# Optimization experiments

Measured on AMD Instinct MI355X. Metric: run time of the kernel, lower is better.

The kernel has to match this reference:

```python
import jax, jax.numpy as jnp
import numpy as np

B, T = 32, 128
D_PATCH, D_PLM, H, P = 128, 768, 4, 64
HD = D_PLM // H          # head_dim = 192
N_TOK = 15               # 1+1+4+4+4+1 patch tokens
EPS = 1e-5


def layernorm(x, g, b):
    m = jnp.mean(x, axis=-1, keepdims=True)
    v = jnp.var(x, axis=-1, keepdims=True)
    return (x - m) * jax.lax.rsqrt(v + EPS) * g + b


def setup_inputs() -> dict:
    key = jax.random.key(0)
    ks = jax.random.split(key, 12)
    nrm = lambda k, shp, s: jax.random.normal(k, shp, jnp.float32) * s
    return {
        "state":    jax.random.normal(ks[0], (B, T, 6, 6), jnp.float32),
        # per-feature patch embedders: scalar feats (0,1,5) in_dim=1, windowed feats (2,3,4) in_dim=3
        "w_scalar": nrm(ks[1], (3, 1, D_PATCH), 0.5),
        "b_scalar": jnp.zeros((3, D_PATCH), jnp.float32),
        "w_patch":  nrm(ks[2], (3, 3, D_PATCH), 0.3),
        "b_patch":  jnp.zeros((3, D_PATCH), jnp.float32),
        "feat_emb": nrm(ks[3], (6, D_PATCH), 0.02),
        "pn_g": jnp.ones((D_PATCH,), jnp.float32),
        "pn_b": jnp.zeros((D_PATCH,), jnp.float32),
        "wq": nrm(ks[4], (D_PATCH, D_PLM), 0.05), "bq": jnp.zeros((D_PLM,), jnp.float32),
        "wk": nrm(ks[5], (D_PLM, D_PLM), 0.02),   "bk": jnp.zeros((D_PLM,), jnp.float32),
        "wv": nrm(ks[6], (D_PLM, D_PLM), 0.02),   "bv": jnp.zeros((D_PLM,), jnp.float32),
        "wp": nrm(ks[7], (D_PATCH, D_PLM), 0.05), "bp": jnp.zeros((D_PLM,), jnp.float32),
        "wo": nrm(ks[8], (D_PLM, D_PLM), 0.02),   "bo": jnp.zeros((D_PLM,), jnp.float32),
        "on_g": jnp.ones((D_PLM,), jnp.float32),
        "on_b": jnp.zeros((D_PLM,), jnp.float32),
        # text prototype bank (rows sampled from word embedding table in the original)
        "protos": nrm(ks[9], (P, D_PLM), 1.0),
    }


def reference(state, w_scalar, b_scalar, w_patch, b_patch, feat_emb, pn_g, pn_b,
              wq, bq, wk, bk, wv, bv, wp, bp, wo, bo, on_g, on_b, protos):
    b, t = state.shape[0], state.shape[1]
    s = state.reshape(b * t, 6, 6)                       # (N,6,6)
    N = s.shape[0]

    # scalar features 0,1,5: last timestep, patch_size=1 -> 1 token each
    sc = s[:, jnp.array([0, 1, 5]), -1]                  # (N,3)
    sc_emb = sc[..., None] * w_scalar[:, 0][None] + b_scalar[None]   # (N,3,Dp)
    sc_emb = sc_emb + feat_emb[jnp.array([0, 1, 5])][None]

    # windowed features 2,3,4: length 6, patch_len 3, stride 1 -> 4 tokens each
    pf = s[:, jnp.array([2, 3, 4]), :]                   # (N,3,6)
    win = jnp.stack([pf[..., i:i + 3] for i in range(4)], axis=2)    # (N,3,4,3)
    p_emb = jnp.einsum('nfkp,fpd->nfkd', win, w_patch) + b_patch[None, :, None]
    p_emb = p_emb + feat_emb[jnp.array([2, 3, 4])][None, :, None]

    # concat in feature order 0,1,2,3,4,5 -> (N,15,Dp), then LayerNorm
    pe = jnp.concatenate([sc_emb[:, 0:1], sc_emb[:, 1:2],
                          p_emb[:, 0], p_emb[:, 1], p_emb[:, 2],
                          sc_emb[:, 2:3]], axis=1)
    pe = layernorm(pe, pn_g, pn_b)

    # cross-attention: Q from patches, K/V from 64 text prototypes
    q = (pe @ wq + bq).reshape(N, N_TOK, H, HD)
    k = (protos @ wk + bk).reshape(P, H, HD)
    v = (protos @ wv + bv).reshape(P, H, HD)
    scores = jnp.einsum('nthd,phd->nhtp', q, k) / np.float32(np.sqrt(HD))
    attn = jax.nn.softmax(scores, axis=-1)               # (N,H,T,P)
    rep = jnp.einsum('nhtp,phd->nthd', attn, v).reshape(N, N_TOK, D_PLM)

    out = (rep @ wo + bo) + (pe @ wp + bp)               # dual projection residual
    out = layernorm(out, on_g, on_b)
    return out.reshape(b, t, N_TOK, D_PLM)
```

## Files before the change

kernel.cpp:

```cpp
#include <hip/hip_runtime.h>

#define NTOK 15
#define DP   128
#define DM   768
#define NH   4
#define HD   192
#define NP   64
#define EPSF 1e-5f
#define KW2  384

typedef __attribute__((ext_vector_type(8))) short bf16x8;
typedef __attribute__((ext_vector_type(4))) float f32x4;
typedef __attribute__((ext_vector_type(4))) unsigned short us4;

__device__ __forceinline__ unsigned short f2bf(float x) {
    unsigned u = __float_as_uint(x);
    u = (u + 0x7FFF + ((u >> 16) & 1)) >> 16;
    return (unsigned short)u;
}
__device__ __forceinline__ int swzP(int row, int b) { return row * 256 + (b ^ ((row & 7) << 4)); }
__device__ __forceinline__ int swzB(int row, int b) { return row * 512 + (b ^ ((row & 7) << 4)); }

__global__ __launch_bounds__(192) void kv_kernel(
    const float* __restrict__ protos,
    const float* __restrict__ wk, const float* __restrict__ bk,
    const float* __restrict__ wv, const float* __restrict__ bv,
    float* __restrict__ Kraw, float* __restrict__ Vf)
{
    int r  = blockIdx.x >> 2;
    int jc = blockIdx.x & 3;
    int j  = jc * 192 + threadIdx.x;
    __shared__ float prow[DM];
    for (int i = threadIdx.x; i < DM; i += 192) prow[i] = protos[r * DM + i];
    __syncthreads();
    float aK = bk[j], aV = bv[j];
    for (int d = 0; d < DM; ++d) {
        float p = prow[d];
        aK += p * wk[d * DM + j];
        aV += p * wv[d * DM + j];
    }
    int h = j / HD, jj = j - h * HD;
    Kraw[(h * NP + r) * HD + jj] = aK;
    Vf[r * DM + j] = aV;
}

__global__ __launch_bounds__(256) void fold_kernel(
    const float* __restrict__ Kraw, const float* __restrict__ Vf,
    const float* __restrict__ wq, const float* __restrict__ bq,
    const float* __restrict__ wo, const float* __restrict__ wp,
    unsigned short* __restrict__ KWb, float* __restrict__ kqb,
    unsigned short* __restrict__ Wcat)
{
    int b = blockIdx.x, tid = threadIdx.x;
    if (b >= 256) {
        int idx = (b - 256) * 256 + tid;
        int j = idx >> 7, d = idx & 127;
        Wcat[(size_t)j * KW2 + 256 + d] = f2bf(wp[d * DM + j]);
        return;
    }
    int hp = b, h = hp >> 6, p = hp & 63;
    __shared__ float Kl[HD], Vl[HD];
    if (tid < HD) {
        Kl[tid] = Kraw[hp * HD + tid];
        Vl[tid] = Vf[p * DM + h * HD + tid];
    }
    __syncthreads();
    const float scale = 0.07216878364870323f;
    if (tid < DP) {
        float a = 0.f;
        for (int l = 0; l < HD; ++l) a += wq[tid * DM + h * HD + l] * Kl[l];
        KWb[hp * DP + tid] = f2bf(scale * a);
    } else if (tid == DP) {
        float a = 0.f;
        for (int l = 0; l < HD; ++l) a += bq[h * HD + l] * Kl[l];
        kqb[hp] = scale * a;
    }
    for (int jj = 0; jj < 3; ++jj) {
        int j = jj * 256 + tid;
        float a = 0.f;
        for (int l = 0; l < HD; ++l) a += wo[(h * HD + l) * DM + j] * Vl[l];
        Wcat[(size_t)j * KW2 + hp] = f2bf(a);
    }
}

__global__ __launch_bounds__(256, 4) void phaseA_kernel(
    const float* __restrict__ state,
    const float* __restrict__ w_scalar, const float* __restrict__ b_scalar,
    const float* __restrict__ w_patch,  const float* __restrict__ b_patch,
    const float* __restrict__ feat_emb,
    const float* __restrict__ pn_g, const float* __restrict__ pn_b,
    const unsigned short* __restrict__ KWb, const float* __restrict__ kqb,
    unsigned short* __restrict__ abufG, int Nrows)
{
    int tid = threadIdx.x;
    int w = tid >> 6, lane = tid & 63;
    int kg = lane >> 4, lr = lane & 15;
    int nb = blockIdx.x;
    size_t rowbase = (size_t)nb * 32;

    __shared__ float peF[32 * DP];
    __shared__ __align__(16) char pebf[32 * 256];
    __shared__ float srow[72];

    if (tid < 72) {
        int rr = tid / 36;
        int gr = nb * 2 + rr;
        srow[tid] = (gr < Nrows) ? state[(size_t)gr * 36 + (tid - rr * 36)] : 0.f;
    }
    __syncthreads();

    #pragma unroll
    for (int it = 0; it < 16; ++it) {
        int idx = it * 256 + tid;
        int row = idx >> 7, d = idx & 127;
        int t = row & 15;
        const float* sr = &srow[(row >> 4) * 36];
        float val;
        if (t == 15) {
            val = 0.f;
        } else if (t == 0) {
            val = sr[5]  * w_scalar[0 * DP + d] + b_scalar[0 * DP + d] + feat_emb[0 * DP + d];
        } else if (t == 1) {
            val = sr[11] * w_scalar[1 * DP + d] + b_scalar[1 * DP + d] + feat_emb[1 * DP + d];
        } else if (t == 14) {
            val = sr[35] * w_scalar[2 * DP + d] + b_scalar[2 * DP + d] + feat_emb[5 * DP + d];
        } else {
            int f = (t - 2) / 4;
            int k = (t - 2) % 4;
            const float* pr = &sr[(2 + f) * 6];
            float acc = b_patch[f * DP + d] + feat_emb[(2 + f) * DP + d];
            for (int p = 0; p < 3; ++p) acc += pr[k + p] * w_patch[(f * 3 + p) * DP + d];
            val = acc;
        }
        peF[row * DP + d] = val;
    }
    __syncthreads();

    {
        int g = tid >> 3, ln = tid & 7;
        int t = g & 15;
        int gr = nb * 2 + (g >> 4);
        if (t == 15 || gr >= Nrows) {
            for (int d = ln; d < DP; d += 8)
                *(unsigned short*)(pebf + swzP(g, d * 2)) = 0;
        } else {
            float s = 0.f, s2 = 0.f;
            for (int d = ln; d < DP; d += 8) { float x = peF[g * DP + d]; s += x; s2 += x * x; }
            for (int off = 4; off; off >>= 1) {
                s  += __shfl_xor(s,  off, 64);
                s2 += __shfl_xor(s2, off, 64);
            }
            float m   = s / DP;
            float var = s2 / DP - m * m;
            float rin = 1.0f / sqrtf(var + EPSF);
            for (int d = ln; d < DP; d += 8) {
                float x = (peF[g * DP + d] - m) * rin * pn_g[d] + pn_b[d];
                *(unsigned short*)(pebf + swzP(g, d * 2)) = f2bf(x);
            }
        }
    }
    __syncthreads();

    {
        const int h = w;
        const unsigned short* kwh = KWb + (size_t)h * NP * DP;
        bf16x8 ka[4][4];
        float4 kqv[4];
        #pragma unroll
        for (int Mt = 0; Mt < 4; ++Mt) {
            #pragma unroll
            for (int kk = 0; kk < 4; ++kk)
                ka[Mt][kk] = *(const bf16x8*)(kwh + (Mt * 16 + lr) * DP + kk * 32 + kg * 8);
            kqv[Mt] = *(const float4*)(kqb + h * 64 + Mt * 16 + kg * 4);
        }
        #pragma unroll
        for (int Ntl = 0; Ntl < 2; ++Ntl) {
            bf16x8 qb[4];
            #pragma unroll
            for (int kk = 0; kk < 4; ++kk)
                qb[kk] = *(const bf16x8*)(pebf + swzP(Ntl * 16 + lr, (kk * 32 + kg * 8) * 2));
            f32x4 sacc[4];
            #pragma unroll
            for (int Mt = 0; Mt < 4; ++Mt) sacc[Mt] = (f32x4){0.f, 0.f, 0.f, 0.f};
            #pragma unroll
            for (int kk = 0; kk < 4; ++kk)
                #pragma unroll
                for (int Mt = 0; Mt < 4; ++Mt)
                    sacc[Mt] = __builtin_amdgcn_mfma_f32_16x16x32_bf16(ka[Mt][kk], qb[kk], sacc[Mt], 0, 0, 0);
            #pragma unroll
            for (int Mt = 0; Mt < 4; ++Mt) {
                sacc[Mt][0] += kqv[Mt].x; sacc[Mt][1] += kqv[Mt].y;
                sacc[Mt][2] += kqv[Mt].z; sacc[Mt][3] += kqv[Mt].w;
            }
            float mx = -3.4e38f;
            #pragma unroll
            for (int Mt = 0; Mt < 4; ++Mt)
                #pragma unroll
                for (int r = 0; r < 4; ++r) mx = fmaxf(mx, sacc[Mt][r]);
            mx = fmaxf(mx, __shfl_xor(mx, 16, 64));
            mx = fmaxf(mx, __shfl_xor(mx, 32, 64));
            float sum = 0.f;
            f32x4 ee[4];
            #pragma unroll
            for (int Mt = 0; Mt < 4; ++Mt)
                #pragma unroll
                for (int r = 0; r < 4; ++r) { float e = __expf(sacc[Mt][r] - mx); ee[Mt][r] = e; sum += e; }
            sum += __shfl_xor(sum, 16, 64);
            sum += __shfl_xor(sum, 32, 64);
            float inv = 1.0f / sum;
            unsigned short* dst = abufG + (rowbase + Ntl * 16 + lr) * KW2 + h * 64 + kg * 4;
            #pragma unroll
            for (int Mt = 0; Mt < 4; ++Mt) {
                us4 v = { f2bf(ee[Mt][0] * inv), f2bf(ee[Mt][1] * inv),
                          f2bf(ee[Mt][2] * inv), f2bf(ee[Mt][3] * inv) };
                *(us4*)(dst + Mt * 16) = v;
            }
        }
    }

    #pragma unroll
    for (int c = 0; c < 2; ++c) {
        int idx = c * 256 + tid;
        int row = idx >> 4, chunk = idx & 15;
        bf16x8 v = *(const bf16x8*)(pebf + swzP(row, chunk * 16));
        *(bf16x8*)(abufG + (rowbase + row) * KW2 + 256 + chunk * 8) = v;
    }
}

__global__ __launch_bounds__(512, 2) void phaseB_kernel(
    const unsigned short* __restrict__ abufG,
    const unsigned short* __restrict__ Wcat,
    const float* __restrict__ bp, const float* __restrict__ bo,
    const float* __restrict__ on_g, const float* __restrict__ on_b,
    float* __restrict__ out, int Nrows)
{
    int tid = threadIdx.x;
    int w = tid >> 6, lane = tid & 63;
    int kg = lane >> 4, lr = lane & 15;
    int nb = blockIdx.x;
    const int n0 = w * 96;

    __shared__ __align__(16) float stage[16 * 772];
    __shared__ float redS[8][64], redS2[8][64];

    const unsigned short* aptr = abufG + (size_t)nb * 64 * KW2;

    float gcol[6], bcol[6];
    f32x4 acc[6][4];
    #pragma unroll
    for (int nt = 0; nt < 6; ++nt) {
        int col = n0 + nt * 16 + lr;
        gcol[nt] = on_g[col]; bcol[nt] = on_b[col];
        float bias = bo[col] + bp[col];
        #pragma unroll
        for (int Mt = 0; Mt < 4; ++Mt) acc[nt][Mt] = (f32x4){bias, bias, bias, bias};
    }

    #pragma unroll
    for (int ks = 0; ks < 12; ++ks) {
        bf16x8 aw[4];
        #pragma unroll
        for (int Mt = 0; Mt < 4; ++Mt)
            aw[Mt] = *(const bf16x8*)(aptr + (Mt * 16 + lr) * KW2 + ks * 32 + kg * 8);
        #pragma unroll
        for (int nt = 0; nt < 6; ++nt) {
            bf16x8 b = *(const bf16x8*)(Wcat + (size_t)(n0 + nt * 16 + lr) * KW2 + ks * 32 + kg * 8);
            #pragma unroll
            for (int Mt = 0; Mt < 4; ++Mt)
                acc[nt][Mt] = __builtin_amdgcn_mfma_f32_16x16x32_bf16(aw[Mt], b, acc[nt][Mt], 0, 0, 0);
        }
    }

    #pragma unroll
    for (int Mt = 0; Mt < 4; ++Mt)
        #pragma unroll
        for (int r = 0; r < 4; ++r) {
            float s = 0.f, q = 0.f;
            #pragma unroll
            for (int nt = 0; nt < 6; ++nt) { float v = acc[nt][Mt][r]; s += v; q += v * v; }
            #pragma unroll
            for (int off = 8; off; off >>= 1) {
                s += __shfl_xor(s, off, 64);
                q += __shfl_xor(q, off, 64);
            }
            if (lr == 0) {
                int tok = Mt * 16 + kg * 4 + r;
                redS [w][tok] = s;
                redS2[w][tok] = q;
            }
        }
    __syncthreads();
    float mA[4][4], riA[4][4];
    #pragma unroll
    for (int Mt = 0; Mt < 4; ++Mt)
        #pragma unroll
        for (int r = 0; r < 4; ++r) {
            int tok = Mt * 16 + kg * 4 + r;
            float ts = 0.f, tq = 0.f;
            #pragma unroll
            for (int ww = 0; ww < 8; ++ww) { ts += redS[ww][tok]; tq += redS2[ww][tok]; }
            float mm  = ts / DM;
            float var = tq / DM - mm * mm;
            mA[Mt][r]  = mm;
            riA[Mt][r] = 1.0f / sqrtf(var + EPSF);
        }

    #pragma unroll
    for (int Mt = 0; Mt < 4; ++Mt) {
        __syncthreads();
        #pragma unroll
        for (int nt = 0; nt < 6; ++nt)
            #pragma unroll
            for (int r = 0; r < 4; ++r)
                stage[(kg * 4 + r) * 772 + n0 + nt * 16 + lr] =
                    (acc[nt][Mt][r] - mA[Mt][r]) * riA[Mt][r] * gcol[nt] + bcol[nt];
        __syncthreads();
        int gr = nb * 4 + Mt;
        if (gr < Nrows) {
            #pragma unroll
            for (int v = 0; v < 6; ++v) {
                int f = v * 512 + tid;
                int row = f / 192, c4 = f - row * 192;
                if (row < NTOK)
                    *(float4*)(out + ((size_t)gr * NTOK + row) * DM + c4 * 4) =
                        *(const float4*)(&stage[row * 772 + c4 * 4]);
            }
        }
    }
}

__global__ __launch_bounds__(512, 4) void row_fused_kernel(
    const float* __restrict__ state,
    const float* __restrict__ w_scalar, const float* __restrict__ b_scalar,
    const float* __restrict__ w_patch,  const float* __restrict__ b_patch,
    const float* __restrict__ feat_emb,
    const float* __restrict__ pn_g, const float* __restrict__ pn_b,
    const unsigned short* __restrict__ KWb, const float* __restrict__ kqb,
    const unsigned short* __restrict__ Wcat,
    const float* __restrict__ bp, const float* __restrict__ bo,
    const float* __restrict__ on_g, const float* __restrict__ on_b,
    float* __restrict__ out, int Nrows)
{
    int tid = threadIdx.x;
    int w = tid >> 6, lane = tid & 63;
    int kg = lane >> 4, lr = lane & 15;
    int nb = blockIdx.x;

    __shared__ __align__(16) char bufA[64 * 512];
    __shared__ __align__(16) char pebf[64 * 256];
    __shared__ float srow[4 * 36];
    __shared__ float redS[8][64], redS2[8][64];

    float* peF = (float*)bufA;

    if (tid < 4 * 36) {
        int rr = tid / 36;
        int gr = nb * 4 + rr;
        srow[tid] = (gr < Nrows) ? state[(size_t)gr * 36 + (tid - rr * 36)] : 0.f;
    }
    __syncthreads();

    for (int idx = tid; idx < 4 * NTOK * DP; idx += 512) {
        int rr  = idx / (NTOK * DP);
        int rem = idx - rr * (NTOK * DP);
        int t = rem >> 7, d = rem & 127;
        const float* sr = &srow[rr * 36];
        float val;
        if (t == 0) {
            val = sr[5]  * w_scalar[0 * DP + d] + b_scalar[0 * DP + d] + feat_emb[0 * DP + d];
        } else if (t == 1) {
            val = sr[11] * w_scalar[1 * DP + d] + b_scalar[1 * DP + d] + feat_emb[1 * DP + d];
        } else if (t == 14) {
            val = sr[35] * w_scalar[2 * DP + d] + b_scalar[2 * DP + d] + feat_emb[5 * DP + d];
        } else {
            int f = (t - 2) / 4;
            int k = (t - 2) % 4;
            const float* pr = &sr[(2 + f) * 6];
            float acc = b_patch[f * DP + d] + feat_emb[(2 + f) * DP + d];
            for (int p = 0; p < 3; ++p) acc += pr[k + p] * w_patch[(f * 3 + p) * DP + d];
            val = acc;
        }
        peF[(rr * 16 + t) * DP + d] = val;
    }
    __syncthreads();

    const int h = w >> 1;
    bf16x8 ka[4][4];
    float4 kqv[4];
    {
        const unsigned short* kwh = KWb + (size_t)h * NP * DP;
        #pragma unroll
        for (int Mt = 0; Mt < 4; ++Mt) {
            #pragma unroll
            for (int kk = 0; kk < 4; ++kk)
                ka[Mt][kk] = *(const bf16x8*)(kwh + (Mt * 16 + lr) * DP + kk * 32 + kg * 8);
            kqv[Mt] = *(const float4*)(kqb + h * 64 + Mt * 16 + kg * 4);
        }
    }

    {
        int g = tid >> 3, ln = tid & 7;
        int t = g & 15;
        int gr = nb * 4 + (g >> 4);
        if (t == 15 || gr >= Nrows) {
            for (int d = ln; d < DP; d += 8)
                *(unsigned short*)(pebf + swzP(g, d * 2)) = 0;
        } else {
            float s = 0.f, s2 = 0.f;
            for (int d = ln; d < DP; d += 8) { float x = peF[g * DP + d]; s += x; s2 += x * x; }
            for (int off = 4; off; off >>= 1) {
                s  += __shfl_xor(s,  off, 64);
                s2 += __shfl_xor(s2, off, 64);
            }
            float m   = s / DP;
            float var = s2 / DP - m * m;
            float rin = 1.0f / sqrtf(var + EPSF);
            for (int d = ln; d < DP; d += 8) {
                float x = (peF[g * DP + d] - m) * rin * pn_g[d] + pn_b[d];
                *(unsigned short*)(pebf + swzP(g, d * 2)) = f2bf(x);
            }
        }
    }
    __syncthreads();

    {
        int Nt0 = (w & 1) * 2;
        #pragma unroll
        for (int Ntl = 0; Ntl < 2; ++Ntl) {
            int Nt = Nt0 + Ntl;
            bf16x8 qb[4];
            #pragma unroll
            for (int kk = 0; kk < 4; ++kk)
                qb[kk] = *(const bf16x8*)(pebf + swzP(Nt * 16 + lr, (kk * 32 + kg * 8) * 2));
            f32x4 sacc[4];
            #pragma unroll
            for (int Mt = 0; Mt < 4; ++Mt) sacc[Mt] = (f32x4){0.f, 0.f, 0.f, 0.f};
            #pragma unroll
            for (int kk = 0; kk < 4; ++kk)
                #pragma unroll
                for (int Mt = 0; Mt < 4; ++Mt)
                    sacc[Mt] = __builtin_amdgcn_mfma_f32_16x16x32_bf16(ka[Mt][kk], qb[kk], sacc[Mt], 0, 0, 0);
            #pragma unroll
            for (int Mt = 0; Mt < 4; ++Mt) {
                sacc[Mt][0] += kqv[Mt].x; sacc[Mt][1] += kqv[Mt].y;
                sacc[Mt][2] += kqv[Mt].z; sacc[Mt][3] += kqv[Mt].w;
            }
            float mx = -3.4e38f;
            #pragma unroll
            for (int Mt = 0; Mt < 4; ++Mt)
                #pragma unroll
                for (int r = 0; r < 4; ++r) mx = fmaxf(mx, sacc[Mt][r]);
            mx = fmaxf(mx, __shfl_xor(mx, 16, 64));
            mx = fmaxf(mx, __shfl_xor(mx, 32, 64));
            float sum = 0.f;
            f32x4 ee[4];
            #pragma unroll
            for (int Mt = 0; Mt < 4; ++Mt)
                #pragma unroll
                for (int r = 0; r < 4; ++r) { float e = __expf(sacc[Mt][r] - mx); ee[Mt][r] = e; sum += e; }
            sum += __shfl_xor(sum, 16, 64);
            sum += __shfl_xor(sum, 32, 64);
            float inv = 1.0f / sum;
            #pragma unroll
            for (int Mt = 0; Mt < 4; ++Mt)
                #pragma unroll
                for (int r = 0; r < 4; ++r) {
                    int c = h * 64 + Mt * 16 + kg * 4 + r;
                    *(unsigned short*)(bufA + swzB(Nt * 16 + lr, c * 2)) = f2bf(ee[Mt][r] * inv);
                }
        }
    }
    __syncthreads();

    const int n0 = w * 96;
    #pragma unroll
    for (int half = 0; half < 2; ++half) {
        f32x4 acc[6][2];
        #pragma unroll
        for (int nt = 0; nt < 6; ++nt) {
            int col = n0 + nt * 16 + lr;
            float bias = bo[col] + bp[col];
            acc[nt][0] = (f32x4){bias, bias, bias, bias};
            acc[nt][1] = (f32x4){bias, bias, bias, bias};
        }
        #pragma unroll
        for (int kkc = 0; kkc < 3; ++kkc) {
            #pragma unroll
            for (int kk = 0; kk < 4; ++kk) {
                bf16x8 aw0, aw1;
                if (kkc < 2) {
                    aw0 = *(const bf16x8*)(bufA + swzB((half * 2 + 0) * 16 + lr, (kkc * 128 + kk * 32 + kg * 8) * 2));
                    aw1 = *(const bf16x8*)(bufA + swzB((half * 2 + 1) * 16 + lr, (kkc * 128 + kk * 32 + kg * 8) * 2));
                } else {
                    aw0 = *(const bf16x8*)(pebf + swzP((half * 2 + 0) * 16 + lr, (kk * 32 + kg * 8) * 2));
                    aw1 = *(const bf16x8*)(pebf + swzP((half * 2 + 1) * 16 + lr, (kk * 32 + kg * 8) * 2));
                }
                int ks = kkc * 4 + kk;
                #pragma unroll
                for (int nt = 0; nt < 6; ++nt) {
                    bf16x8 b = *(const bf16x8*)(Wcat + (size_t)(n0 + nt * 16 + lr) * KW2 + ks * 32 + kg * 8);
                    acc[nt][0] = __builtin_amdgcn_mfma_f32_16x16x32_bf16(aw0, b, acc[nt][0], 0, 0, 0);
                    acc[nt][1] = __builtin_amdgcn_mfma_f32_16x16x32_bf16(aw1, b, acc[nt][1], 0, 0, 0);
                }
            }
        }
        #pragma unroll
        for (int Mtl = 0; Mtl < 2; ++Mtl)
            #pragma unroll
            for (int r = 0; r < 4; ++r) {
                float s = 0.f, q = 0.f;
                #pragma unroll
                for (int nt = 0; nt < 6; ++nt) { float v = acc[nt][Mtl][r]; s += v; q += v * v; }
                #pragma unroll
                for (int off = 8; off; off >>= 1) {
                    s += __shfl_xor(s, off, 64);
                    q += __shfl_xor(q, off, 64);
                }
                if (lr == 0) {
                    int tok = (half * 2 + Mtl) * 16 + kg * 4 + r;
                    redS [w][tok] = s;
                    redS2[w][tok] = q;
                }
            }
        __syncthreads();
        #pragma unroll
        for (int Mtl = 0; Mtl < 2; ++Mtl) {
            float mA[4], riA[4];
            #pragma unroll
            for (int r = 0; r < 4; ++r) {
                int tok = (half * 2 + Mtl) * 16 + kg * 4 + r;
                float ts = 0.f, tq = 0.f;
                #pragma unroll
                for (int ww = 0; ww < 8; ++ww) { ts += redS[ww][tok]; tq += redS2[ww][tok]; }
                float mm  = ts / DM;
                float var = tq / DM - mm * mm;
                mA[r]  = mm;
                riA[r] = 1.0f / sqrtf(var + EPSF);
            }
            #pragma unroll
            for (int nt = 0; nt < 6; ++nt) {
                int col = n0 + nt * 16 + lr;
                float g = on_g[col], bb = on_b[col];
                #pragma unroll
                for (int r = 0; r < 4; ++r) {
                    int tok = (half * 2 + Mtl) * 16 + kg * 4 + r;
                    int t = tok & 15, rr = tok >> 4;
                    int gr = nb * 4 + rr;
                    if (t < NTOK && gr < Nrows)
                        out[((size_t)gr * NTOK + t) * DM + col] =
                            (acc[nt][Mtl][r] - mA[r]) * riA[r] * g + bb;
                }
            }
        }
    }
}

extern "C" void kernel_launch(void* const* d_in, const int* in_sizes, int n_in,
                              void* d_out, int out_size, void* d_ws, size_t ws_size,
                              hipStream_t stream) {
    const float* state    = (const float*)d_in[0];
    const float* w_scalar = (const float*)d_in[1];
    const float* b_scalar = (const float*)d_in[2];
    const float* w_patch  = (const float*)d_in[3];
    const float* b_patch  = (const float*)d_in[4];
    const float* feat_emb = (const float*)d_in[5];
    const float* pn_g     = (const float*)d_in[6];
    const float* pn_b     = (const float*)d_in[7];
    const float* wq       = (const float*)d_in[8];
    const float* bq       = (const float*)d_in[9];
    const float* wk       = (const float*)d_in[10];
    const float* bk       = (const float*)d_in[11];
    const float* wv       = (const float*)d_in[12];
    const float* bv       = (const float*)d_in[13];
    const float* wp       = (const float*)d_in[14];
    const float* bp       = (const float*)d_in[15];
    const float* wo       = (const float*)d_in[16];
    const float* bo       = (const float*)d_in[17];
    const float* on_g     = (const float*)d_in[18];
    const float* on_b     = (const float*)d_in[19];
    const float* protos   = (const float*)d_in[20];
    float* out = (float*)d_out;

    float*          Kraw = (float*)d_ws;
    float*          Vf   = Kraw + 256 * HD;
    float*          kqbp = Vf + NP * DM;
    unsigned short* KWb  = (unsigned short*)(kqbp + 256);
    unsigned short* Wcat = KWb + 256 * DP;
    unsigned short* abufG = Wcat + (size_t)DM * KW2;

    int N = in_sizes[0] / 36;
    int nblkA = (N + 1) / 2;
    int nblkB = (N + 3) / 4;
    size_t tokrows = (size_t)nblkB * 64;
    size_t need = 1049600ull + tokrows * KW2 * 2ull;

    hipLaunchKernelGGL(kv_kernel, dim3(256), dim3(192), 0, stream,
                       protos, wk, bk, wv, bv, Kraw, Vf);
    hipLaunchKernelGGL(fold_kernel, dim3(640), dim3(256), 0, stream,
                       Kraw, Vf, wq, bq, wo, wp, KWb, kqbp, Wcat);

    if (ws_size >= need) {
        hipLaunchKernelGGL(phaseA_kernel, dim3(nblkA), dim3(256), 0, stream,
                           state, w_scalar, b_scalar, w_patch, b_patch, feat_emb,
                           pn_g, pn_b, KWb, kqbp, abufG, N);
        hipLaunchKernelGGL(phaseB_kernel, dim3(nblkB), dim3(512), 0, stream,
                           abufG, Wcat, bp, bo, on_g, on_b, out, N);
    } else {
        hipLaunchKernelGGL(row_fused_kernel, dim3(nblkB), dim3(512), 0, stream,
                           state, w_scalar, b_scalar, w_patch, b_patch, feat_emb,
                           pn_g, pn_b, KWb, kqbp, Wcat, bp, bo, on_g, on_b,
                           out, N);
    }
}
```

Measured before the change: 297.1 us.

## Stage phaseB A-tile in swizzled LDS via direct global-to-LDS loads

New measurement: 429.6 us. 1.45x slower.

```diff
diff --git a/kernel.cpp b/kernel.cpp
--- a/kernel.cpp
+++ b/kernel.cpp
@@ -208,12 +208,13 @@
             sum += __shfl_xor(sum, 16, 64);
             sum += __shfl_xor(sum, 32, 64);
             float inv = 1.0f / sum;
-            unsigned short* dst = abufG + (rowbase + Ntl * 16 + lr) * KW2 + h * 64 + kg * 4;
+            char* rowp = (char*)abufG + (rowbase + Ntl * 16 + lr) * 768;
+            int swz = (lr & 7) << 4;
             #pragma unroll
             for (int Mt = 0; Mt < 4; ++Mt) {
                 us4 v = { f2bf(ee[Mt][0] * inv), f2bf(ee[Mt][1] * inv),
                           f2bf(ee[Mt][2] * inv), f2bf(ee[Mt][3] * inv) };
-                *(us4*)(dst + Mt * 16) = v;
+                *(us4*)(rowp + ((h * 128 + Mt * 32 + kg * 8) ^ swz)) = v;
             }
         }
     }
@@ -223,11 +224,12 @@
         int idx = c * 256 + tid;
         int row = idx >> 4, chunk = idx & 15;
         bf16x8 v = *(const bf16x8*)(pebf + swzP(row, chunk * 16));
-        *(bf16x8*)(abufG + (rowbase + row) * KW2 + 256 + chunk * 8) = v;
+        *(bf16x8*)((char*)abufG + (rowbase + row) * 768 +
+                   ((512 + chunk * 16) ^ ((row & 7) << 4))) = v;
     }
 }
 
-__global__ __launch_bounds__(512, 2) void phaseB_kernel(
+__global__ __launch_bounds__(512, 4) void phaseB_kernel(
     const unsigned short* __restrict__ abufG,
     const unsigned short* __restrict__ Wcat,
     const float* __restrict__ bp, const float* __restrict__ bo,
@@ -240,10 +242,19 @@
     int nb = blockIdx.x;
     const int n0 = w * 96;
 
-    __shared__ __align__(16) float stage[16 * 772];
+    __shared__ __align__(16) char lds_raw[49152];
     __shared__ float redS[8][64], redS2[8][64];
 
-    const unsigned short* aptr = abufG + (size_t)nb * 64 * KW2;
+    {
+        const char* src = (const char*)abufG + (size_t)nb * 64 * 768;
+        #pragma unroll
+        for (int s = 0; s < 6; ++s) {
+            __builtin_amdgcn_global_load_lds(
+                (const __attribute__((address_space(1))) unsigned int*)(src + s * 8192 + tid * 16),
+                (__attribute__((address_space(3))) unsigned int*)(lds_raw + s * 8192 + tid * 16),
+                16, 0, 0);
+        }
+    }
 
     float gcol[6], bcol[6];
     f32x4 acc[6][4];
@@ -256,12 +267,18 @@
         for (int Mt = 0; Mt < 4; ++Mt) acc[nt][Mt] = (f32x4){bias, bias, bias, bias};
     }
 
+    asm volatile("s_waitcnt vmcnt(0)");
+    __syncthreads();
+
     #pragma unroll
     for (int ks = 0; ks < 12; ++ks) {
         bf16x8 aw[4];
         #pragma unroll
-        for (int Mt = 0; Mt < 4; ++Mt)
-            aw[Mt] = *(const bf16x8*)(aptr + (Mt * 16 + lr) * KW2 + ks * 32 + kg * 8);
+        for (int Mt = 0; Mt < 4; ++Mt) {
+            int row = Mt * 16 + lr;
+            aw[Mt] = *(const bf16x8*)(lds_raw + row * 768 +
+                                      ((ks * 64 + kg * 16) ^ ((row & 7) << 4)));
+        }
         #pragma unroll
         for (int nt = 0; nt < 6; ++nt) {
             bf16x8 b = *(const bf16x8*)(Wcat + (size_t)(n0 + nt * 16 + lr) * KW2 + ks * 32 + kg * 8);
@@ -305,25 +322,32 @@
             riA[Mt][r] = 1.0f / sqrtf(var + EPSF);
         }
 
+    float* stage = (float*)lds_raw;
     #pragma unroll
     for (int Mt = 0; Mt < 4; ++Mt) {
-        __syncthreads();
-        #pragma unroll
-        for (int nt = 0; nt < 6; ++nt)
-            #pragma unroll
-            for (int r = 0; r < 4; ++r)
-                stage[(kg * 4 + r) * 772 + n0 + nt * 16 + lr] =
-                    (acc[nt][Mt][r] - mA[Mt][r]) * riA[Mt][r] * gcol[nt] + bcol[nt];
-        __syncthreads();
         int gr = nb * 4 + Mt;
-        if (gr < Nrows) {
-            #pragma unroll
-            for (int v = 0; v < 6; ++v) {
-                int f = v * 512 + tid;
-                int row = f / 192, c4 = f - row * 192;
-                if (row < NTOK)
-                    *(float4*)(out + ((size_t)gr * NTOK + row) * DM + c4 * 4) =
-                        *(const float4*)(&stage[row * 772 + c4 * 4]);
+        #pragma unroll
+        for (int hh = 0; hh < 2; ++hh) {
+            __syncthreads();
+            if ((kg >> 1) == hh) {
+                #pragma unroll
+                for (int nt = 0; nt < 6; ++nt)
+                    #pragma unroll
+                    for (int r = 0; r < 4; ++r)
+                        stage[((kg & 1) * 4 + r) * 772 + n0 + nt * 16 + lr] =
+                            (acc[nt][Mt][r] - mA[Mt][r]) * riA[Mt][r] * gcol[nt] + bcol[nt];
+            }
+            __syncthreads();
+            if (gr < Nrows) {
+                #pragma unroll
+                for (int v = 0; v < 3; ++v) {
+                    int f = v * 512 + tid;
+                    int row8 = f / 192, c4 = f - row8 * 192;
+                    int tok = hh * 8 + row8;
+                    if (tok < NTOK)
+                        *(float4*)(out + ((size_t)gr * NTOK + tok) * DM + c4 * 4) =
+                            *(const float4*)(&stage[row8 * 772 + c4 * 4]);
+                }
             }
         }
     }
```
